# Optimization experiments

Measured on AMD Instinct MI355X. Metric: run time of the kernel, lower is better.

Reference implementation:

```python
import jax, jax.numpy as jnp
import numpy as np


def setup_inputs() -> dict:
    key = jax.random.key(0)
    k1, k2 = jax.random.split(key)
    B, N, M, D = 32, 2048, 2048, 3
    x = jax.random.normal(k1, (B, N, D), dtype=jnp.float32)
    y = jax.random.normal(k2, (B, M, D), dtype=jnp.float32)
    return {"x": x, "y": y}


def reference(x, y):
    # x: [B, N, D], y: [B, M, D]
    # dist[b, m, n] = ||x[b, n] - y[b, m]||^2  -> [B, M, N]
    diff = x[:, None, :, :] - y[:, :, None, :]          # [B, M, N, D]
    dist = jnp.sum(diff * diff, axis=-1)                # [B, M, N]
    # min over M (axis 1): for each x-point, nearest y-point; mean over N
    row = jnp.mean(jnp.min(dist, axis=1), axis=-1)      # [B]
    # min over N (axis 2): for each y-point, nearest x-point; mean over M
    col = jnp.mean(jnp.min(dist, axis=2), axis=-1)      # [B]
    # per-batch max of the two directed means, then mean over batch
    return jnp.mean(jnp.maximum(row, col))
```

## Files before the change

kernel.cpp:

```cpp
#include <hip/hip_runtime.h>


#define BATCH   32
#define NPTS    2048
#define THREADS 256
#define QPT     8
#define TCH     32
#define TC      (NPTS / TCH)
#define NSEG    (2 * BATCH)
#define CBLK    8
#define NCOMB   (NSEG * CBLK)

__global__ __launch_bounds__(THREADS) void chamfer_min(
    const float* __restrict__ x, const float* __restrict__ y,
    float* __restrict__ part ,
    unsigned* __restrict__ done)
{
    __shared__ float4 t4[TC];

    const int blk   = blockIdx.x;
    const int dir   = blk >> 10;
    const int r     = blk & 1023;
    const int b     = r >> 5;
    const int chunk = r & 31;

    if (blk == 0 && threadIdx.x == 0) *done = 0u;

    const float* q = (dir == 0 ? x : y) + (size_t)b * NPTS * 3;
    const float* t = (dir == 0 ? y : x) + (size_t)b * NPTS * 3;

    if (threadIdx.x < TC) {
        int jj = chunk * TC + threadIdx.x;
        float tx = t[3 * jj + 0];
        float ty = t[3 * jj + 1];
        float tz = t[3 * jj + 2];
        t4[threadIdx.x] = make_float4(tx, ty, tz, 0.5f * (tx * tx + ty * ty + tz * tz));
    }

    float qx[QPT], qy[QPT], qz[QPT], mn[QPT];
#pragma unroll
    for (int k = 0; k < QPT; ++k) {
        int qi = threadIdx.x + k * THREADS;
        qx[k] = q[3 * qi + 0];
        qy[k] = q[3 * qi + 1];
        qz[k] = q[3 * qi + 2];
        mn[k] = 3.4e38f;
    }
    __syncthreads();

#pragma unroll 4
    for (int j = 0; j < TC; j += 2) {
        float4 a = t4[j];
        float4 c = t4[j + 1];
#pragma unroll
        for (int k = 0; k < QPT; ++k) {
            float s0 = fmaf(-qz[k], a.z, fmaf(-qy[k], a.y, fmaf(-qx[k], a.x, a.w)));
            float s1 = fmaf(-qz[k], c.z, fmaf(-qy[k], c.y, fmaf(-qx[k], c.x, c.w)));
            mn[k] = fminf(fminf(mn[k], s0), s1);
        }
    }

    float* pbase = part + ((size_t)(dir * BATCH + b) * TCH + chunk) * NPTS;
#pragma unroll
    for (int k = 0; k < QPT; ++k)
        pbase[threadIdx.x + k * THREADS] = mn[k];
}

__global__ __launch_bounds__(THREADS) void chamfer_combine(
    const float* __restrict__ x, const float* __restrict__ y,
    const float* __restrict__ part,
    float* __restrict__ blocksums ,
    unsigned* __restrict__ done,
    float* __restrict__ out)
{
    __shared__ float wsum[THREADS / 64];
    __shared__ int flagLast;

    const int blk = blockIdx.x;
    const int seg = blk >> 3;
    const int qc  = blk & 7;
    const int dir = seg >> 5;
    const int b   = seg & 31;
    const int qi  = qc * THREADS + threadIdx.x;

    const float* p = part + (size_t)seg * TCH * NPTS + qi;
    float mn = p[0];
#pragma unroll
    for (int c = 1; c < TCH; ++c)
        mn = fminf(mn, p[(size_t)c * NPTS]);

    const float* q = (dir == 0 ? x : y) + (size_t)b * NPTS * 3 + 3 * qi;
    float qx = q[0], qy = q[1], qz = q[2];
    float d = fmaf(2.0f, mn, qx * qx + qy * qy + qz * qz);

    for (int off = 32; off > 0; off >>= 1)
        d += __shfl_down(d, off);
    if ((threadIdx.x & 63) == 0) wsum[threadIdx.x >> 6] = d;
    __syncthreads();

    if (threadIdx.x == 0) {
        float tot = wsum[0] + wsum[1] + wsum[2] + wsum[3];
        __hip_atomic_store(&blocksums[blk], tot, __ATOMIC_RELEASE,
                           __HIP_MEMORY_SCOPE_AGENT);
        unsigned old = __hip_atomic_fetch_add(done, 1u, __ATOMIC_ACQ_REL,
                                              __HIP_MEMORY_SCOPE_AGENT);
        flagLast = (old == (unsigned)(NCOMB - 1));
    }
    __syncthreads();
    if (!flagLast) return;

    if (threadIdx.x < 64) {
        const int lane = threadIdx.x;
        float s = 0.0f;
#pragma unroll
        for (int i = 0; i < CBLK; ++i)
            s += __hip_atomic_load(&blocksums[lane * CBLK + i],
                                   __ATOMIC_ACQUIRE, __HIP_MEMORY_SCOPE_AGENT);
        float other = __shfl(s, lane + 32);
        float v = (lane < 32) ? fmaxf(s, other) * (1.0f / NPTS) : 0.0f;
        for (int off = 16; off > 0; off >>= 1)
            v += __shfl_down(v, off);
        if (lane == 0) out[0] = v * (1.0f / BATCH);
    }
}

extern "C" void kernel_launch(void* const* d_in, const int* in_sizes, int n_in,
                              void* d_out, int out_size, void* d_ws, size_t ws_size,
                              hipStream_t stream) {
    const float* x = (const float*)d_in[0];
    const float* y = (const float*)d_in[1];
    float* out = (float*)d_out;

    float*    part      = (float*)d_ws;
    float*    blocksums = part + (size_t)NSEG * TCH * NPTS;
    unsigned* done      = (unsigned*)(blocksums + NCOMB);

    chamfer_min<<<2 * BATCH * TCH, THREADS, 0, stream>>>(x, y, part, done);
    chamfer_combine<<<NCOMB, THREADS, 0, stream>>>(x, y, part, blocksums, done, out);
}
```

Before: 96.24 us.

## Prepack points as float4 with half-norm and read targets from global memory

Adds a pre-pass kernel that packs every point of x and y into a float4 holding coordinates and half the squared norm. The min kernel then reads query and target points directly from this packed buffer, dropping the shared-memory staging and its barrier. Target chunks are halved in count (TCH 32 to 16), which doubles the work per block and shrinks the partial-min buffer. The combine kernel reuses the precomputed norm. The cost is an extra kernel launch, and the inner loop now issues uniform global loads instead of LDS reads.

```diff
diff --git a/kernel.cpp b/kernel.cpp
--- a/kernel.cpp
+++ b/kernel.cpp
@@ -5,57 +5,59 @@
 #define NPTS    2048
 #define THREADS 256
 #define QPT     8
-#define TCH     32
+#define TCH     16
 #define TC      (NPTS / TCH)
 #define NSEG    (2 * BATCH)
 #define CBLK    8
 #define NCOMB   (NSEG * CBLK)
+#define NPTSTOT (2 * BATCH * NPTS)
+
+__global__ __launch_bounds__(THREADS) void chamfer_pack(
+    const float* __restrict__ x, const float* __restrict__ y,
+    float4* __restrict__ packed, unsigned* __restrict__ done)
+{
+    const int gid = blockIdx.x * THREADS + threadIdx.x;
+    if (gid == 0) *done = 0u;
+    const int dir = gid >> 16;
+    const int idx = gid & 0xFFFF;
+    const float* src = (dir == 0 ? y : x);
+    float px = src[3 * idx + 0];
+    float py = src[3 * idx + 1];
+    float pz = src[3 * idx + 2];
+    packed[gid] = make_float4(px, py, pz, 0.5f * (px * px + py * py + pz * pz));
+}
 
 __global__ __launch_bounds__(THREADS) void chamfer_min(
-    const float* __restrict__ x, const float* __restrict__ y,
-    float* __restrict__ part ,
-    unsigned* __restrict__ done)
+    const float4* __restrict__ packed,
+    float* __restrict__ part )
 {
-    __shared__ float4 t4[TC];
+    const int blk   = blockIdx.x;
+    const int dir   = blk >> 9;
+    const int r     = blk & 511;
+    const int b     = r >> 4;
+    const int chunk = r & 15;
 
-    const int blk   = blockIdx.x;
-    const int dir   = blk >> 10;
-    const int r     = blk & 1023;
-    const int b     = r >> 5;
-    const int chunk = r & 31;
+    const float4* tq = packed + ((size_t)dir << 16) + b * NPTS + chunk * TC;
+    const float4* qq = packed + ((size_t)(1 - dir) << 16) + b * NPTS;
 
-    if (blk == 0 && threadIdx.x == 0) *done = 0u;
-
-    const float* q = (dir == 0 ? x : y) + (size_t)b * NPTS * 3;
-    const float* t = (dir == 0 ? y : x) + (size_t)b * NPTS * 3;
-
-    if (threadIdx.x < TC) {
-        int jj = chunk * TC + threadIdx.x;
-        float tx = t[3 * jj + 0];
-        float ty = t[3 * jj + 1];
-        float tz = t[3 * jj + 2];
-        t4[threadIdx.x] = make_float4(tx, ty, tz, 0.5f * (tx * tx + ty * ty + tz * tz));
-    }
-
-    float qx[QPT], qy[QPT], qz[QPT], mn[QPT];
+    float nqx[QPT], nqy[QPT], nqz[QPT], mn[QPT];
 #pragma unroll
     for (int k = 0; k < QPT; ++k) {
-        int qi = threadIdx.x + k * THREADS;
-        qx[k] = q[3 * qi + 0];
-        qy[k] = q[3 * qi + 1];
-        qz[k] = q[3 * qi + 2];
-        mn[k] = 3.4e38f;
+        float4 qv = qq[threadIdx.x + k * THREADS];
+        nqx[k] = -qv.x;
+        nqy[k] = -qv.y;
+        nqz[k] = -qv.z;
+        mn[k]  = 3.4e38f;
     }
-    __syncthreads();
 
 #pragma unroll 4
     for (int j = 0; j < TC; j += 2) {
-        float4 a = t4[j];
-        float4 c = t4[j + 1];
+        float4 a = tq[j];
+        float4 c = tq[j + 1];
 #pragma unroll
         for (int k = 0; k < QPT; ++k) {
-            float s0 = fmaf(-qz[k], a.z, fmaf(-qy[k], a.y, fmaf(-qx[k], a.x, a.w)));
-            float s1 = fmaf(-qz[k], c.z, fmaf(-qy[k], c.y, fmaf(-qx[k], c.x, c.w)));
+            float s0 = fmaf(nqz[k], a.z, fmaf(nqy[k], a.y, fmaf(nqx[k], a.x, a.w)));
+            float s1 = fmaf(nqz[k], c.z, fmaf(nqy[k], c.y, fmaf(nqx[k], c.x, c.w)));
             mn[k] = fminf(fminf(mn[k], s0), s1);
         }
     }
@@ -67,7 +69,7 @@
 }
 
 __global__ __launch_bounds__(THREADS) void chamfer_combine(
-    const float* __restrict__ x, const float* __restrict__ y,
+    const float4* __restrict__ packed,
     const float* __restrict__ part,
     float* __restrict__ blocksums ,
     unsigned* __restrict__ done,
@@ -89,9 +91,8 @@
     for (int c = 1; c < TCH; ++c)
         mn = fminf(mn, p[(size_t)c * NPTS]);
 
-    const float* q = (dir == 0 ? x : y) + (size_t)b * NPTS * 3 + 3 * qi;
-    float qx = q[0], qy = q[1], qz = q[2];
-    float d = fmaf(2.0f, mn, qx * qx + qy * qy + qz * qz);
+    float4 qv = packed[((size_t)(1 - dir) << 16) + b * NPTS + qi];
+    float d = 2.0f * (mn + qv.w);
 
     for (int off = 32; off > 0; off >>= 1)
         d += __shfl_down(d, off);
@@ -131,10 +132,13 @@
     const float* y = (const float*)d_in[1];
     float* out = (float*)d_out;
 
-    float*    part      = (float*)d_ws;
-    float*    blocksums = part + (size_t)NSEG * TCH * NPTS;
+    char* ws = (char*)d_ws;
+    float*    part      = (float*)ws;
+    float4*   packed    = (float4*)(ws + (size_t)NSEG * TCH * NPTS * 4);
+    float*    blocksums = (float*)(packed + NPTSTOT);
     unsigned* done      = (unsigned*)(blocksums + NCOMB);
 
-    chamfer_min<<<2 * BATCH * TCH, THREADS, 0, stream>>>(x, y, part, done);
-    chamfer_combine<<<NCOMB, THREADS, 0, stream>>>(x, y, part, blocksums, done, out);
+    chamfer_pack<<<NPTSTOT / THREADS, THREADS, 0, stream>>>(x, y, packed, done);
+    chamfer_min<<<2 * BATCH * TCH, THREADS, 0, stream>>>(packed, part);
+    chamfer_combine<<<NCOMB, THREADS, 0, stream>>>(packed, part, blocksums, done, out);
 }
```

After: 105.2 us. 9.3% more time.
